# Optimization experiments

Measured on AMD Instinct MI355X. Metric: run time of the kernel, lower is better.

Reference implementation:

```python
import jax, jax.numpy as jnp
import numpy as np

B, S, D, H = 4, 2048, 1024, 16
DH = D // H
NEG = -100000.0


def setup_inputs() -> dict:
    key = jax.random.key(0)
    ks = jax.random.split(key, 13)
    s = 1.0 / np.sqrt(D)
    inp = {
        'q': jax.random.normal(ks[0], (B, S, D), jnp.float32),
        'k': jax.random.normal(ks[1], (B, S, D), jnp.float32),
        'v': jax.random.normal(ks[2], (B, S, D), jnp.float32),
        'mask': jax.random.randint(ks[3], (B, 1, S, S), 0, 2).astype(bool),
        'wq_w': jax.random.normal(ks[4], (D, D), jnp.float32) * s,
        'wq_b': jnp.zeros((D,), jnp.float32),
        'wk_w': jax.random.normal(ks[5], (D, D), jnp.float32) * s,
        'wk_b': jnp.zeros((D,), jnp.float32),
        'wv_w': jax.random.normal(ks[6], (D, D), jnp.float32) * s,
        'wv_b': jnp.zeros((D,), jnp.float32),
        'wo_w': jax.random.normal(ks[7], (D, D), jnp.float32) * s,
        'wo_b': jnp.zeros((D,), jnp.float32),
    }
    return inp


def reference(q, k, v, mask, wq_w, wq_b, wk_w, wk_b, wv_w, wv_b, wo_w, wo_b):
    # torch Linear: y = x @ W^T + b
    qh = (q @ wq_w.T + wq_b).reshape(B, S, H, DH).transpose(0, 2, 1, 3)  # [B,H,S,DH]
    kh = (k @ wk_w.T + wk_b).reshape(B, S, H, DH).transpose(0, 2, 1, 3)
    vh = (v @ wv_w.T + wv_b).reshape(B, S, H, DH).transpose(0, 2, 1, 3)
    # NOTE: original code has NO 1/sqrt(d) scaling
    alpha = jnp.einsum('bhqd,bhkd->bhqk', qh, kh)  # [B,H,S,S]
    alpha = jnp.where(mask, NEG, alpha)
    score = jax.nn.softmax(alpha, axis=-1)
    x = jnp.einsum('bhqk,bhkd->bhqd', score, vh)
    x = x.transpose(0, 2, 1, 3).reshape(B, S, D)
    return x @ wo_w.T + wo_b
```

## Files before the change

### kernel.cpp

```cpp
#include <hip/hip_runtime.h>
#include <hip/hip_bf16.h>

#define B_ 4
#define S_ 2048
#define D_ 1024
#define H_ 16
#define NEGV (-100000.0f)
#define L2E 1.4426950408889634f

typedef __attribute__((ext_vector_type(8))) short short8;
typedef __attribute__((ext_vector_type(4))) float f32x4;
typedef _Float16 hf2 __attribute__((ext_vector_type(2)));
typedef unsigned short us;
typedef unsigned long long u64;

__device__ __forceinline__ us f2h(float f) {
  union { _Float16 h; us u; } c;
  c.h = (_Float16)f;
  return c.u;
}
__device__ __forceinline__ float exp2a(float x) {
  float r;
  asm("v_exp_f32 %0, %1" : "=v"(r) : "v"(x));
  return r;
}

__global__ void detect_mask_kernel(const int* __restrict__ mi, int* __restrict__ flag) {
  int t = threadIdx.x;
  bool bad = false;
  for (int i = t; i < 16384; i += 64) {
    int v = mi[i];
    bad = bad || (v != 0 && v != 1);
  }
  unsigned long long any = __ballot(bad);
  if (t == 0) flag[0] = (any != 0ull) ? 1 : 0;
}

__global__ __launch_bounds__(256) void pack_mask(const void* __restrict__ maskp,
                                                 const int* __restrict__ flag,
                                                 unsigned* __restrict__ pk) {
  int w = blockIdx.x * 256 + threadIdx.x;
  unsigned bits = 0;
  if (flag[0]) {
    const uint4* p = (const uint4*)((const unsigned char*)maskp + (size_t)w * 32);
#pragma unroll
    for (int q = 0; q < 2; ++q) {
      uint4 v = p[q];
      unsigned vv[4] = {v.x, v.y, v.z, v.w};
#pragma unroll
      for (int e = 0; e < 4; ++e) {
        unsigned byte4 = vv[e];
#pragma unroll
        for (int bb = 0; bb < 4; ++bb)
          bits |= (unsigned)(((byte4 >> (8 * bb)) & 0xffu) != 0) << (q * 16 + e * 4 + bb);
      }
    }
  } else {
    const uint4* p = (const uint4*)((const int*)maskp + (size_t)w * 32);
#pragma unroll
    for (int q = 0; q < 8; ++q) {
      uint4 v = p[q];
      bits |= (unsigned)(v.x != 0) << (q * 4 + 0);
      bits |= (unsigned)(v.y != 0) << (q * 4 + 1);
      bits |= (unsigned)(v.z != 0) << (q * 4 + 2);
      bits |= (unsigned)(v.w != 0) << (q * 4 + 3);
    }
  }
  pk[w] = bits;
}

__global__ __launch_bounds__(256) void cvt_f16x3(const float* __restrict__ i0,
                                                 const float* __restrict__ i1,
                                                 const float* __restrict__ i2,
                                                 us* __restrict__ o0, us* __restrict__ o1,
                                                 us* __restrict__ o2) {
  int z = blockIdx.x >> 12;
  int i = (blockIdx.x & 4095) * 256 + threadIdx.x;
  const float* in = z == 0 ? i0 : z == 1 ? i1 : i2;
  us* out = z == 0 ? o0 : z == 1 ? o1 : o2;
  float4 a = ((const float4*)in)[2 * i];
  float4 b = ((const float4*)in)[2 * i + 1];
  us u[8] = {f2h(a.x), f2h(a.y), f2h(a.z), f2h(a.w),
             f2h(b.x), f2h(b.y), f2h(b.z), f2h(b.w)};
  ((uint4*)out)[i] = *(uint4*)u;
}

__global__ __launch_bounds__(256) void cvt_w4(const float* __restrict__ w0,
                                              const float* __restrict__ w1,
                                              const float* __restrict__ w2,
                                              const float* __restrict__ w3,
                                              us* __restrict__ d0, us* __restrict__ d1,
                                              us* __restrict__ d2, us* __restrict__ d3) {
  int which = blockIdx.x >> 9;
  int i = (blockIdx.x & 511) * 256 + threadIdx.x;
  const float* w = which == 0 ? w0 : which == 1 ? w1 : which == 2 ? w2 : w3;
  us* d = which == 0 ? d0 : which == 1 ? d1 : which == 2 ? d2 : d3;
  float4 a = ((const float4*)w)[2 * i];
  float4 b = ((const float4*)w)[2 * i + 1];
  us u[8] = {f2h(a.x), f2h(a.y), f2h(a.z), f2h(a.w),
             f2h(b.x), f2h(b.y), f2h(b.z), f2h(b.w)};
  ((uint4*)d)[i] = *(uint4*)u;
}

__device__ __forceinline__ void gload16(const us* g, us* l) {
  __builtin_amdgcn_global_load_lds((const __attribute__((address_space(1))) void*)g,
                                   (__attribute__((address_space(3))) void*)l, 16, 0, 0);
}

__device__ __forceinline__ int swzb(int row, int c16) {
  return row * 128 + ((c16 ^ (row & 7)) << 4);
}

template <int OMODE>
__global__ __launch_bounds__(256) void gemm_mfma(
    const us* __restrict__ A0, const us* __restrict__ A1, const us* __restrict__ A2,
    const us* __restrict__ Wp0, const us* __restrict__ Wp1, const us* __restrict__ Wp2,
    const float* __restrict__ b0, const float* __restrict__ b1, const float* __restrict__ b2,
    void* __restrict__ C0, void* __restrict__ C1, void* __restrict__ C2,
    int M, int N, int K, int trans_z) {
  __shared__ __align__(16) us SM[32768];

  const int z = blockIdx.z;
  const us* A = z == 0 ? A0 : z == 1 ? A1 : A2;
  const us* W = z == 0 ? Wp0 : z == 1 ? Wp1 : Wp2;
  const float* bias = z == 0 ? b0 : z == 1 ? b1 : b2;
  void* Cp = z == 0 ? C0 : z == 1 ? C1 : C2;

  const int m0 = blockIdx.x * 128;
  const int n0 = blockIdx.y * 128;
  const int t = threadIdx.x;
  const int w = t >> 6, l = t & 63;
  const int l15 = l & 15, l4 = l >> 4;
  const int wm = w >> 1, wn = w & 1;

  int goff[4];
#pragma unroll
  for (int j = 0; j < 4; ++j) {
    int u = t + j * 256;
    int r = u >> 3, c8 = u & 7;
    int g = c8 ^ (r & 7);
    goff[j] = r * K + g * 8;
  }
  const us* Ag = A + (size_t)m0 * K;
  const us* Wg = W + (size_t)n0 * K;

  f32x4 acc[4][4];
#pragma unroll
  for (int m = 0; m < 4; ++m)
#pragma unroll
    for (int n = 0; n < 4; ++n) acc[m][n] = (f32x4){0.f, 0.f, 0.f, 0.f};

  auto stage = [&](int k0, int bb) {
#pragma unroll
    for (int j = 0; j < 4; ++j) {
      int u = t + j * 256;
      gload16(Ag + goff[j] + k0, SM + bb * 8192 + u * 8);
      gload16(Wg + goff[j] + k0, SM + 16384 + bb * 8192 + u * 8);
    }
  };

  stage(0, 0);
  __syncthreads();
  int cur = 0;
  for (int k0 = 0; k0 < K; k0 += 64) {
    if (k0 + 64 < K) stage(k0 + 64, cur ^ 1);
#pragma unroll
    for (int ks = 0; ks < 2; ++ks) {
      short8 ah[4], bh_[4];
#pragma unroll
      for (int m = 0; m < 4; ++m)
        ah[m] = *(const short8*)((const char*)(SM + cur * 8192) +
                                 swzb(wm * 64 + m * 16 + l15, ks * 4 + l4));
#pragma unroll
      for (int n = 0; n < 4; ++n)
        bh_[n] = *(const short8*)((const char*)(SM + 16384 + cur * 8192) +
                                  swzb(wn * 64 + n * 16 + l15, ks * 4 + l4));
#pragma unroll
      for (int m = 0; m < 4; ++m)
#pragma unroll
        for (int n = 0; n < 4; ++n)
          acc[m][n] = __builtin_amdgcn_mfma_f32_16x16x32_f16(ah[m], bh_[n], acc[m][n], 0, 0, 0);
    }
    __syncthreads();
    cur ^= 1;
  }

  float bv[4];
#pragma unroll
  for (int n = 0; n < 4; ++n) bv[n] = bias[n0 + wn * 64 + n * 16 + l15];

  if (OMODE == 2 && z == trans_z) {
    us* T = SM;
#pragma unroll
    for (int n = 0; n < 4; ++n) {
      int col = wn * 64 + n * 16 + l15;
#pragma unroll
      for (int m = 0; m < 4; ++m) {
        int sr = wm * 64 + m * 16 + l4 * 4;
#pragma unroll
        for (int ip = 0; ip < 2; ++ip) {
          us h0 = f2h(acc[m][n][2 * ip] + bv[n]);
          us h1 = f2h(acc[m][n][2 * ip + 1] + bv[n]);
          *(unsigned*)&T[col * 136 + sr + 2 * ip] = (unsigned)h0 | ((unsigned)h1 << 16);
        }
      }
    }
    __syncthreads();
    const int b = m0 >> 11, sb = m0 & (S_ - 1);
    const int colr = t >> 1, sc = (t & 1) << 6;
    const int hh = (n0 >> 6) + (colr >> 6), d = colr & 63;
    us* dst = (us*)Cp + (((size_t)(b * H_ + hh) << 6) + (size_t)d) * S_ + sb + sc;
#pragma unroll
    for (int p = 0; p < 8; ++p)
      *(uint4*)(dst + p * 8) = *(const uint4*)&T[colr * 136 + sc + p * 8];
    return;
  }

#pragma unroll
  for (int m = 0; m < 4; ++m) {
#pragma unroll
    for (int i = 0; i < 4; ++i) {
      int gm = m0 + wm * 64 + m * 16 + l4 * 4 + i;
#pragma unroll
      for (int n = 0; n < 4; ++n) {
        int gn = n0 + wn * 64 + n * 16 + l15;
        float o = acc[m][n][i] + bv[n];
        if constexpr (OMODE == 0) {
          ((float*)Cp)[(size_t)gm * N + gn] = o;
        } else {
          int b = gm >> 11, s = gm & (S_ - 1);
          int hh = gn >> 6, d = gn & 63;
          size_t idx = (((size_t)(b * H_ + hh) << 11) + s) * 64 + d;
          ((us*)Cp)[idx] = f2h(o);
        }
      }
    }
  }
}

__device__ __forceinline__ int swz(int row, int bc) {
  return (row << 7) + (bc ^ ((row & 7) << 4));
}

__global__ __launch_bounds__(512) void attn_mfma(
    const us* __restrict__ qh, const us* __restrict__ kh,
    const us* __restrict__ vt, const unsigned* __restrict__ pk,
    us* __restrict__ xout) {
  __shared__ __align__(16) us Ks[2][4096];
  __shared__ __align__(16) us Vs[2][4096];
  __shared__ __align__(16) char Ps[16384];
  __shared__ __align__(16) float MLutF[64];

  const int blk = ((blockIdx.x & 7) << 7) + (blockIdx.x >> 3);
  const int bh = blk >> 4;
  const int q0 = (blk & 15) << 7;
  const int b = bh >> 4, h = bh & (H_ - 1);
  const int t = threadIdx.x;
  const int w = t >> 6, l = t & 63;
  const int l15 = l & 15, l4 = l >> 4;

  short8 qf[2];
  {
    const size_t qbase = ((size_t)bh * S_ + q0 + 16 * w + l15) * 64 + l4 * 8;
    qf[0] = *(const short8*)(qh + qbase);
    qf[1] = *(const short8*)(qh + qbase + 32);
  }

  f32x4 accO[4];
#pragma unroll
  for (int jd = 0; jd < 4; ++jd) accO[jd] = (f32x4){0.f, 0.f, 0.f, 0.f};
  float m_i = -1e30f, l_p = 0.f;

  const int r_st = t >> 3, c_st = (t & 7) ^ ((t >> 3) & 7);
  const us* kh_src = kh + ((size_t)bh * S_ + r_st) * 64 + c_st * 8;
  const us* vt_src = vt + ((size_t)bh * 64 + r_st) * S_ + c_st * 8;

  auto stage = [&](int k0, int bb) {
    gload16(kh_src + (size_t)k0 * 64, &Ks[bb][t * 8]);
    gload16(vt_src + k0, &Vs[bb][t * 8]);
  };

  if (t < 64) MLutF[t] = (((t >> 2) >> (t & 3)) & 1) ? NEGV : 0.f;
  stage(0, 0);
  __syncthreads();
  int cur = 0;

  char* Pw = Ps + w * 2048;
  const int prowb = l15 * 128;
  const int rr7 = l15 & 7;
  const int bhalf = l4 >> 1;
  const int wsub = (l4 & 1) * 8;
  const unsigned* pb = pk + ((size_t)b * S_ + q0 + 16 * w + l15) * (S_ / 32);

  for (int k0 = 0; k0 < S_; k0 += 64) {
    uint2 mw = *(const uint2*)(pb + (k0 >> 5));
    if (k0 + 64 < S_) stage(k0 + 64, cur ^ 1);

    const char* KT = (const char*)Ks[cur];
    const char* VT = (const char*)Vs[cur];

    __builtin_amdgcn_s_setprio(1);
    f32x4 sj[4];
#pragma unroll
    for (int j = 0; j < 4; ++j) {
      f32x4 s = {0.f, 0.f, 0.f, 0.f};
#pragma unroll
      for (int c = 0; c < 2; ++c) {
        short8 kf = *(const short8*)(KT + swz(l15 + 16 * j, l4 * 16 + 64 * c));
        s = __builtin_amdgcn_mfma_f32_16x16x32_f16(kf, qf[c], s, 0, 0, 0);
      }
      sj[j] = s;
    }
    __builtin_amdgcn_s_setprio(0);

#pragma unroll
    for (int j = 0; j < 4; ++j) {
      unsigned wrd = (j < 2) ? mw.x : mw.y;
      unsigned nib = (wrd >> (((j & 1) << 4) + (l4 << 2))) & 0xFu;
      f32x4 lv = *(const f32x4*)&MLutF[nib << 2];
      sj[j] = sj[j] + lv;
    }

    float c0 = fmaxf(fmaxf(sj[0][0], sj[0][1]), sj[0][2]);
    float c1 = fmaxf(fmaxf(sj[0][3], sj[1][0]), sj[1][1]);
    float c2 = fmaxf(fmaxf(sj[1][2], sj[1][3]), sj[2][0]);
    float c3 = fmaxf(fmaxf(sj[2][1], sj[2][2]), sj[2][3]);
    float c4 = fmaxf(fmaxf(sj[3][0], sj[3][1]), sj[3][2]);
    float tm = fmaxf(fmaxf(fmaxf(c0, c1), c2), fmaxf(fmaxf(c3, c4), sj[3][3]));
    tm = fmaxf(tm, __shfl_xor(tm, 16));
    tm = fmaxf(tm, __shfl_xor(tm, 32));

    if (__any(tm - m_i > 8.0f)) {
      float mnew = fmaxf(m_i, tm);
      float scl = exp2a((m_i - mnew) * L2E);
      l_p *= scl;
      m_i = mnew;
      float sr0 = __shfl(scl, 4 * l4 + 0);
      float sr1 = __shfl(scl, 4 * l4 + 1);
      float sr2 = __shfl(scl, 4 * l4 + 2);
      float sr3 = __shfl(scl, 4 * l4 + 3);
#pragma unroll
      for (int jd = 0; jd < 4; ++jd) {
        accO[jd][0] *= sr0; accO[jd][1] *= sr1;
        accO[jd][2] *= sr2; accO[jd][3] *= sr3;
      }
    }

    float ml2 = m_i * L2E;
    hf2 acc2;
    acc2.x = (_Float16)0.f;
    acc2.y = (_Float16)0.f;
#pragma unroll
    for (int j = 0; j < 4; ++j) {
      float p0 = exp2a(fmaf(sj[j][0], L2E, -ml2));
      float p1 = exp2a(fmaf(sj[j][1], L2E, -ml2));
      float p2 = exp2a(fmaf(sj[j][2], L2E, -ml2));
      float p3 = exp2a(fmaf(sj[j][3], L2E, -ml2));
      unsigned d0, d1;
      asm("v_cvt_pkrtz_f16_f32 %0, %1, %2" : "=v"(d0) : "v"(p0), "v"(p1));
      asm("v_cvt_pkrtz_f16_f32 %0, %1, %2" : "=v"(d1) : "v"(p2), "v"(p3));
      union { unsigned u; hf2 h; } c0u, c1u;
      c0u.u = d0;
      c1u.u = d1;
      acc2 = acc2 + c0u.h + c1u.h;
      int chunk = ((j << 1) | bhalf) ^ rr7;
      *(u64*)(Pw + prowb + (chunk << 4) + wsub) = (u64)d0 | ((u64)d1 << 32);
    }
    l_p += (float)acc2.x + (float)acc2.y;
    asm volatile("s_waitcnt lgkmcnt(0)" ::: "memory");
    __builtin_amdgcn_sched_barrier(0);

    __builtin_amdgcn_s_setprio(1);
#pragma unroll
    for (int kc = 0; kc < 2; ++kc) {
      int chR = (4 * kc + l4) ^ rr7;
      short8 pa = *(const short8*)(Pw + prowb + (chR << 4));
#pragma unroll
      for (int jd = 0; jd < 4; ++jd) {
        short8 vb = *(const short8*)(VT + swz(l15 + 16 * jd, l4 * 16 + 64 * kc));
        accO[jd] = __builtin_amdgcn_mfma_f32_16x16x32_f16(pa, vb, accO[jd], 0, 0, 0);
      }
    }
    __builtin_amdgcn_s_setprio(0);
    __syncthreads();
    cur ^= 1;
  }

  float lr = l_p;
  lr += __shfl_xor(lr, 16);
  lr += __shfl_xor(lr, 32);
  float inv0 = 1.f / __shfl(lr, 4 * l4 + 0);
  float inv1 = 1.f / __shfl(lr, 4 * l4 + 1);
  float inv2 = 1.f / __shfl(lr, 4 * l4 + 2);
  float inv3 = 1.f / __shfl(lr, 4 * l4 + 3);
  float invs[4] = {inv0, inv1, inv2, inv3};
#pragma unroll
  for (int i = 0; i < 4; ++i) {
    int row = q0 + 16 * w + l4 * 4 + i;
    size_t obase = ((size_t)b * S_ + row) * D_ + h * 64 + l15;
#pragma unroll
    for (int jd = 0; jd < 4; ++jd) xout[obase + 16 * jd] = f2h(accO[jd][i] * invs[i]);
  }
}

extern "C" void kernel_launch(void* const* d_in, const int* in_sizes, int n_in,
                              void* d_out, int out_size, void* d_ws, size_t ws_size,
                              hipStream_t stream) {
  const float* q = (const float*)d_in[0];
  const float* k = (const float*)d_in[1];
  const float* v = (const float*)d_in[2];
  const void* mask = d_in[3];
  const float* wq_w = (const float*)d_in[4];
  const float* wq_b = (const float*)d_in[5];
  const float* wk_w = (const float*)d_in[6];
  const float* wk_b = (const float*)d_in[7];
  const float* wv_w = (const float*)d_in[8];
  const float* wv_b = (const float*)d_in[9];
  const float* wo_w = (const float*)d_in[10];
  const float* wo_b = (const float*)d_in[11];

  const size_t NE = (size_t)B_ * S_ * D_;
  const size_t NW = (size_t)D_ * D_;
  const size_t PKB = (size_t)(B_ * S_ * (S_ / 32)) * 4;
  char* ws = (char*)d_ws;
  int* flag = (int*)ws;
  unsigned* pkb = (unsigned*)(ws + 256);
  us* base = (us*)(ws + 256 + PKB);

  detect_mask_kernel<<<1, 64, 0, stream>>>((const int*)mask, flag);
  pack_mask<<<2048, 256, 0, stream>>>(mask, flag, pkb);

  dim3 g2(64, 8, 2);
  dim3 g3(64, 8, 3);
  dim3 g1(64, 8, 1);

  const size_t fused_need = 256 + PKB + 6 * NE * 2 + 4 * NW * 2;
  if (ws_size >= fused_need) {
    us* A0 = base;
    us* A1 = A0 + NE;
    us* A2 = A1 + NE;
    us* A3 = A2 + NE;
    us* A4 = A3 + NE;
    us* A5 = A4 + NE;
    us* W0 = A5 + NE;
    us* W1 = W0 + NW;
    us* W2 = W1 + NW;
    us* W3 = W2 + NW;
    cvt_w4<<<2048, 256, 0, stream>>>(wq_w, wk_w, wv_w, wo_w, W0, W1, W2, W3);
    cvt_f16x3<<<3 * 4096, 256, 0, stream>>>(q, k, v, A0, A1, A2);
    gemm_mfma<2><<<g3, 256, 0, stream>>>(A0, A1, A2, W0, W1, W2, wq_b, wk_b, wv_b,
                                         A3, A4, A5, B_ * S_, D_, D_, 2);
    attn_mfma<<<1024, 512, 0, stream>>>(A3, A4, A5, pkb, A0);
    gemm_mfma<0><<<g1, 256, 0, stream>>>(A0, A0, A0, W3, W3, W3, wo_b, wo_b, wo_b,
                                         d_out, d_out, d_out, B_ * S_, D_, D_, -1);
  } else {
    us* A0 = base;
    us* A1 = A0 + NE;
    us* A2 = A1 + NE;
    us* A3 = A2 + NE;
    us* A4 = A3 + NE;
    us* W0 = A4 + NE;
    us* W1 = W0 + NW;
    us* W2 = W1 + NW;
    us* W3 = W2 + NW;
    cvt_w4<<<2048, 256, 0, stream>>>(wq_w, wk_w, wv_w, wo_w, W0, W1, W2, W3);
    cvt_f16x3<<<2 * 4096, 256, 0, stream>>>(q, k, nullptr, A0, A1, nullptr);
    gemm_mfma<2><<<g2, 256, 0, stream>>>(A0, A1, nullptr, W0, W1, nullptr, wq_b, wk_b, nullptr,
                                         A2, A3, nullptr, B_ * S_, D_, D_, -1);
    cvt_f16x3<<<4096, 256, 0, stream>>>(v, nullptr, nullptr, A0, nullptr, nullptr);
    gemm_mfma<2><<<g1, 256, 0, stream>>>(A0, nullptr, nullptr, W2, nullptr, nullptr,
                                         wv_b, nullptr, nullptr, A4, nullptr, nullptr,
                                         B_ * S_, D_, D_, 0);
    attn_mfma<<<1024, 512, 0, stream>>>(A2, A3, A4, pkb, A0);
    gemm_mfma<0><<<g1, 256, 0, stream>>>(A0, nullptr, nullptr, W3, nullptr, nullptr,
                                         wo_b, nullptr, nullptr, d_out, nullptr, nullptr,
                                         B_ * S_, D_, D_, -1);
  }
}
```

Before: 346.6 us.

## Deepen GEMM pipeline to four stages and merge prep launches

The projection GEMM now uses a 4-deep ring of 32-wide K tiles, with explicit vmcnt waits and raw barriers instead of a double-buffered 64-wide loop. This keeps more global-to-LDS loads in flight, and the smaller LDS footprint plus launch_bounds(256,2) aims for two blocks per CU. Mask detection is merged into the weight-conversion kernel and mask packing into the input-conversion kernel, which cuts the launch count. The hand-written waitcnt counts depend on the exact number of loads per stage, so they are fragile, and each tile now takes more barriers.

```diff
diff --git a/kernel.cpp b/kernel.cpp
--- a/kernel.cpp
+++ b/kernel.cpp
@@ -36,12 +36,9 @@
   if (t == 0) flag[0] = (any != 0ull) ? 1 : 0;
 }
 
-__global__ __launch_bounds__(256) void pack_mask(const void* __restrict__ maskp,
-                                                 const int* __restrict__ flag,
-                                                 unsigned* __restrict__ pk) {
-  int w = blockIdx.x * 256 + threadIdx.x;
+__device__ __forceinline__ unsigned pack_words(const void* maskp, int mode, int w) {
   unsigned bits = 0;
-  if (flag[0]) {
+  if (mode) {
     const uint4* p = (const uint4*)((const unsigned char*)maskp + (size_t)w * 32);
 #pragma unroll
     for (int q = 0; q < 2; ++q) {
@@ -66,7 +63,22 @@
       bits |= (unsigned)(v.w != 0) << (q * 4 + 3);
     }
   }
-  pk[w] = bits;
+  return bits;
+}
+
+__global__ __launch_bounds__(256) void pack_mask(const void* __restrict__ maskp,
+                                                 const int* __restrict__ flag,
+                                                 unsigned* __restrict__ pk) {
+  int w = blockIdx.x * 256 + threadIdx.x;
+  pk[w] = pack_words(maskp, flag[0], w);
+}
+
+__device__ __forceinline__ void cvt8(const float* in, us* out, int i) {
+  float4 a = ((const float4*)in)[2 * i];
+  float4 b = ((const float4*)in)[2 * i + 1];
+  us u[8] = {f2h(a.x), f2h(a.y), f2h(a.z), f2h(a.w),
+             f2h(b.x), f2h(b.y), f2h(b.z), f2h(b.w)};
+  ((uint4*)out)[i] = *(uint4*)u;
 }
 
 __global__ __launch_bounds__(256) void cvt_f16x3(const float* __restrict__ i0,
@@ -78,28 +90,48 @@
   int i = (blockIdx.x & 4095) * 256 + threadIdx.x;
   const float* in = z == 0 ? i0 : z == 1 ? i1 : i2;
   us* out = z == 0 ? o0 : z == 1 ? o1 : o2;
-  float4 a = ((const float4*)in)[2 * i];
-  float4 b = ((const float4*)in)[2 * i + 1];
-  us u[8] = {f2h(a.x), f2h(a.y), f2h(a.z), f2h(a.w),
-             f2h(b.x), f2h(b.y), f2h(b.z), f2h(b.w)};
-  ((uint4*)out)[i] = *(uint4*)u;
-}
-
-__global__ __launch_bounds__(256) void cvt_w4(const float* __restrict__ w0,
-                                              const float* __restrict__ w1,
-                                              const float* __restrict__ w2,
-                                              const float* __restrict__ w3,
-                                              us* __restrict__ d0, us* __restrict__ d1,
-                                              us* __restrict__ d2, us* __restrict__ d3) {
+  cvt8(in, out, i);
+}
+
+__global__ __launch_bounds__(256) void prep_w(
+    const float* __restrict__ w0, const float* __restrict__ w1,
+    const float* __restrict__ w2, const float* __restrict__ w3,
+    us* __restrict__ d0, us* __restrict__ d1, us* __restrict__ d2, us* __restrict__ d3,
+    const int* __restrict__ mi, int* __restrict__ flag) {
+  if (blockIdx.x == 2048) {
+    int t = threadIdx.x;
+    if (t >= 64) return;
+    bool bad = false;
+    for (int i = t; i < 16384; i += 64) {
+      int v = mi[i];
+      bad = bad || (v != 0 && v != 1);
+    }
+    unsigned long long any = __ballot(bad);
+    if (t == 0) flag[0] = (any != 0ull) ? 1 : 0;
+    return;
+  }
   int which = blockIdx.x >> 9;
   int i = (blockIdx.x & 511) * 256 + threadIdx.x;
   const float* w = which == 0 ? w0 : which == 1 ? w1 : which == 2 ? w2 : w3;
   us* d = which == 0 ? d0 : which == 1 ? d1 : which == 2 ? d2 : d3;
-  float4 a = ((const float4*)w)[2 * i];
-  float4 b = ((const float4*)w)[2 * i + 1];
-  us u[8] = {f2h(a.x), f2h(a.y), f2h(a.z), f2h(a.w),
-             f2h(b.x), f2h(b.y), f2h(b.z), f2h(b.w)};
-  ((uint4*)d)[i] = *(uint4*)u;
+  cvt8(w, d, i);
+}
+
+__global__ __launch_bounds__(256) void prep_in(
+    const void* __restrict__ maskp, const int* __restrict__ flag, unsigned* __restrict__ pk,
+    const float* __restrict__ i0, const float* __restrict__ i1, const float* __restrict__ i2,
+    us* __restrict__ o0, us* __restrict__ o1, us* __restrict__ o2) {
+  if (blockIdx.x < 2048) {
+    int w = blockIdx.x * 256 + threadIdx.x;
+    pk[w] = pack_words(maskp, flag[0], w);
+    return;
+  }
+  int c = blockIdx.x - 2048;
+  int z = c >> 12;
+  int i = (c & 4095) * 256 + threadIdx.x;
+  const float* in = z == 0 ? i0 : z == 1 ? i1 : i2;
+  us* out = z == 0 ? o0 : z == 1 ? o1 : o2;
+  cvt8(in, out, i);
 }
 
 __device__ __forceinline__ void gload16(const us* g, us* l) {
@@ -107,18 +139,14 @@
                                    (__attribute__((address_space(3))) void*)l, 16, 0, 0);
 }
 
-__device__ __forceinline__ int swzb(int row, int c16) {
-  return row * 128 + ((c16 ^ (row & 7)) << 4);
-}
-
 template <int OMODE>
-__global__ __launch_bounds__(256) void gemm_mfma(
+__global__ __launch_bounds__(256, 2) void gemm_dp(
     const us* __restrict__ A0, const us* __restrict__ A1, const us* __restrict__ A2,
     const us* __restrict__ Wp0, const us* __restrict__ Wp1, const us* __restrict__ Wp2,
     const float* __restrict__ b0, const float* __restrict__ b1, const float* __restrict__ b2,
     void* __restrict__ C0, void* __restrict__ C1, void* __restrict__ C2,
     int M, int N, int K, int trans_z) {
-  __shared__ __align__(16) us SM[32768];
+  __shared__ __align__(16) us SM[4][8192];
 
   const int z = blockIdx.z;
   const us* A = z == 0 ? A0 : z == 1 ? A1 : A2;
@@ -133,12 +161,12 @@
   const int l15 = l & 15, l4 = l >> 4;
   const int wm = w >> 1, wn = w & 1;
 
-  int goff[4];
-#pragma unroll
-  for (int j = 0; j < 4; ++j) {
+  int goff[2];
+#pragma unroll
+  for (int j = 0; j < 2; ++j) {
     int u = t + j * 256;
-    int r = u >> 3, c8 = u & 7;
-    int g = c8 ^ (r & 7);
+    int r = u >> 2, c4 = u & 3;
+    int g = c4 ^ (r & 3);
     goff[j] = r * K + g * 8;
   }
   const us* Ag = A + (size_t)m0 * K;
@@ -150,47 +178,70 @@
 #pragma unroll
     for (int n = 0; n < 4; ++n) acc[m][n] = (f32x4){0.f, 0.f, 0.f, 0.f};
 
-  auto stage = [&](int k0, int bb) {
-#pragma unroll
-    for (int j = 0; j < 4; ++j) {
+  auto stage = [&](int kt, int bb) {
+#pragma unroll
+    for (int j = 0; j < 2; ++j) {
       int u = t + j * 256;
-      gload16(Ag + goff[j] + k0, SM + bb * 8192 + u * 8);
-      gload16(Wg + goff[j] + k0, SM + 16384 + bb * 8192 + u * 8);
+      gload16(Ag + goff[j] + kt * 32, &SM[bb][u * 8]);
+    }
+#pragma unroll
+    for (int j = 0; j < 2; ++j) {
+      int u = t + j * 256;
+      gload16(Wg + goff[j] + kt * 32, &SM[bb][4096 + u * 8]);
     }
   };
 
+  auto body = [&](int bb) {
+    const char* Ab = (const char*)&SM[bb][0];
+    const char* Bb = Ab + 8192;
+    short8 bf[4], af[4];
+#pragma unroll
+    for (int n = 0; n < 4; ++n) {
+      int row = wn * 64 + n * 16 + l15;
+      bf[n] = *(const short8*)(Bb + row * 64 + ((l4 ^ (row & 3)) << 4));
+    }
+#pragma unroll
+    for (int m = 0; m < 4; ++m) {
+      int row = wm * 64 + m * 16 + l15;
+      af[m] = *(const short8*)(Ab + row * 64 + ((l4 ^ (row & 3)) << 4));
+    }
+#pragma unroll
+    for (int m = 0; m < 4; ++m)
+#pragma unroll
+      for (int n = 0; n < 4; ++n)
+        acc[m][n] = __builtin_amdgcn_mfma_f32_16x16x32_f16(af[m], bf[n], acc[m][n], 0, 0, 0);
+  };
+
+  const int nt = K / 32;
   stage(0, 0);
-  __syncthreads();
-  int cur = 0;
-  for (int k0 = 0; k0 < K; k0 += 64) {
-    if (k0 + 64 < K) stage(k0 + 64, cur ^ 1);
-#pragma unroll
-    for (int ks = 0; ks < 2; ++ks) {
-      short8 ah[4], bh_[4];
-#pragma unroll
-      for (int m = 0; m < 4; ++m)
-        ah[m] = *(const short8*)((const char*)(SM + cur * 8192) +
-                                 swzb(wm * 64 + m * 16 + l15, ks * 4 + l4));
-#pragma unroll
-      for (int n = 0; n < 4; ++n)
-        bh_[n] = *(const short8*)((const char*)(SM + 16384 + cur * 8192) +
-                                  swzb(wn * 64 + n * 16 + l15, ks * 4 + l4));
-#pragma unroll
-      for (int m = 0; m < 4; ++m)
-#pragma unroll
-        for (int n = 0; n < 4; ++n)
-          acc[m][n] = __builtin_amdgcn_mfma_f32_16x16x32_f16(ah[m], bh_[n], acc[m][n], 0, 0, 0);
-    }
+  stage(1, 1);
+  stage(2, 2);
+  int tt = 0;
+  for (; tt < nt - 3; ++tt) {
+    asm volatile("s_waitcnt vmcnt(8)" ::: "memory");
+    asm volatile("s_barrier" ::: "memory");
+    stage(tt + 3, (tt + 3) & 3);
+    body(tt & 3);
+  }
+  asm volatile("s_waitcnt vmcnt(8)" ::: "memory");
+  asm volatile("s_barrier" ::: "memory");
+  body(tt & 3);
+  ++tt;
+  asm volatile("s_waitcnt vmcnt(4)" ::: "memory");
+  asm volatile("s_barrier" ::: "memory");
+  body(tt & 3);
+  ++tt;
+  asm volatile("s_waitcnt vmcnt(0)" ::: "memory");
+  asm volatile("s_barrier" ::: "memory");
+  body(tt & 3);
+
+  float bv[4];
+#pragma unroll
+  for (int n = 0; n < 4; ++n) bv[n] = bias[n0 + wn * 64 + n * 16 + l15];
+
+  if (OMODE == 2 && z == trans_z) {
     __syncthreads();
-    cur ^= 1;
-  }
-
-  float bv[4];
-#pragma unroll
-  for (int n = 0; n < 4; ++n) bv[n] = bias[n0 + wn * 64 + n * 16 + l15];
-
-  if (OMODE == 2 && z == trans_z) {
-    us* T = SM;
+    us* T = (us*)SM;
 #pragma unroll
     for (int n = 0; n < 4; ++n) {
       int col = wn * 64 + n * 16 + l15;
@@ -427,11 +478,8 @@
   unsigned* pkb = (unsigned*)(ws + 256);
   us* base = (us*)(ws + 256 + PKB);
 
-  detect_mask_kernel<<<1, 64, 0, stream>>>((const int*)mask, flag);
-  pack_mask<<<2048, 256, 0, stream>>>(mask, flag, pkb);
-
+  dim3 g3(64, 8, 3);
   dim3 g2(64, 8, 2);
-  dim3 g3(64, 8, 3);
   dim3 g1(64, 8, 1);
 
   const size_t fused_need = 256 + PKB + 6 * NE * 2 + 4 * NW * 2;
@@ -446,13 +494,14 @@
     us* W1 = W0 + NW;
     us* W2 = W1 + NW;
     us* W3 = W2 + NW;
-    cvt_w4<<<2048, 256, 0, stream>>>(wq_w, wk_w, wv_w, wo_w, W0, W1, W2, W3);
-    cvt_f16x3<<<3 * 4096, 256, 0, stream>>>(q, k, v, A0, A1, A2);
-    gemm_mfma<2><<<g3, 256, 0, stream>>>(A0, A1, A2, W0, W1, W2, wq_b, wk_b, wv_b,
-                                         A3, A4, A5, B_ * S_, D_, D_, 2);
+    prep_w<<<2049, 256, 0, stream>>>(wq_w, wk_w, wv_w, wo_w, W0, W1, W2, W3,
+                                     (const int*)mask, flag);
+    prep_in<<<2048 + 3 * 4096, 256, 0, stream>>>(mask, flag, pkb, q, k, v, A0, A1, A2);
+    gemm_dp<2><<<g3, 256, 0, stream>>>(A0, A1, A2, W0, W1, W2, wq_b, wk_b, wv_b,
+                                       A3, A4, A5, B_ * S_, D_, D_, 2);
     attn_mfma<<<1024, 512, 0, stream>>>(A3, A4, A5, pkb, A0);
-    gemm_mfma<0><<<g1, 256, 0, stream>>>(A0, A0, A0, W3, W3, W3, wo_b, wo_b, wo_b,
-                                         d_out, d_out, d_out, B_ * S_, D_, D_, -1);
+    gemm_dp<0><<<g1, 256, 0, stream>>>(A0, A0, A0, W3, W3, W3, wo_b, wo_b, wo_b,
+                                       d_out, d_out, d_out, B_ * S_, D_, D_, -1);
   } else {
     us* A0 = base;
     us* A1 = A0 + NE;
@@ -463,17 +512,20 @@
     us* W1 = W0 + NW;
     us* W2 = W1 + NW;
     us* W3 = W2 + NW;
-    cvt_w4<<<2048, 256, 0, stream>>>(wq_w, wk_w, wv_w, wo_w, W0, W1, W2, W3);
+    detect_mask_kernel<<<1, 64, 0, stream>>>((const int*)mask, flag);
+    pack_mask<<<2048, 256, 0, stream>>>(mask, flag, pkb);
+    prep_w<<<2048, 256, 0, stream>>>(wq_w, wk_w, wv_w, wo_w, W0, W1, W2, W3,
+                                     (const int*)mask, flag);
     cvt_f16x3<<<2 * 4096, 256, 0, stream>>>(q, k, nullptr, A0, A1, nullptr);
-    gemm_mfma<2><<<g2, 256, 0, stream>>>(A0, A1, nullptr, W0, W1, nullptr, wq_b, wk_b, nullptr,
-                                         A2, A3, nullptr, B_ * S_, D_, D_, -1);
+    gemm_dp<2><<<g2, 256, 0, stream>>>(A0, A1, nullptr, W0, W1, nullptr, wq_b, wk_b, nullptr,
+                                       A2, A3, nullptr, B_ * S_, D_, D_, -1);
     cvt_f16x3<<<4096, 256, 0, stream>>>(v, nullptr, nullptr, A0, nullptr, nullptr);
-    gemm_mfma<2><<<g1, 256, 0, stream>>>(A0, nullptr, nullptr, W2, nullptr, nullptr,
-                                         wv_b, nullptr, nullptr, A4, nullptr, nullptr,
-                                         B_ * S_, D_, D_, 0);
+    gemm_dp<2><<<g1, 256, 0, stream>>>(A0, nullptr, nullptr, W2, nullptr, nullptr,
+                                       wv_b, nullptr, nullptr, A4, nullptr, nullptr,
+                                       B_ * S_, D_, D_, 0);
     attn_mfma<<<1024, 512, 0, stream>>>(A2, A3, A4, pkb, A0);
-    gemm_mfma<0><<<g1, 256, 0, stream>>>(A0, nullptr, nullptr, W3, nullptr, nullptr,
-                                         wo_b, nullptr, nullptr, d_out, nullptr, nullptr,
-                                         B_ * S_, D_, D_, -1);
-  }
-}
+    gemm_dp<0><<<g1, 256, 0, stream>>>(A0, nullptr, nullptr, W3, nullptr, nullptr,
+                                       wo_b, nullptr, nullptr, d_out, nullptr, nullptr,
+                                       B_ * S_, D_, D_, -1);
+  }
+}
```

After: 359.5 us. 3.7% more time.

## Merge prep kernels into fewer launches and enlarge attention blocks to 1024 threads

Applied to the files above, without the earlier changes.

Mask detection now runs inside the weight-conversion kernel, and mask packing is fused with the activation conversion, which removes two kernel launches and their serialization. The attention kernel now uses 1024-thread blocks covering 256 query rows. K and V staging is split across the two halves of the block, so each K/V tile in LDS is shared by twice as many query rows. The larger block raises LDS use and register pressure per block, which may lower occupancy, and it halves the grid to 512 blocks.

```diff
diff --git a/kernel.cpp b/kernel.cpp
--- a/kernel.cpp
+++ b/kernel.cpp
@@ -36,12 +36,9 @@
   if (t == 0) flag[0] = (any != 0ull) ? 1 : 0;
 }
 
-__global__ __launch_bounds__(256) void pack_mask(const void* __restrict__ maskp,
-                                                 const int* __restrict__ flag,
-                                                 unsigned* __restrict__ pk) {
-  int w = blockIdx.x * 256 + threadIdx.x;
+__device__ __forceinline__ unsigned pack_words(const void* maskp, int mode, int w) {
   unsigned bits = 0;
-  if (flag[0]) {
+  if (mode) {
     const uint4* p = (const uint4*)((const unsigned char*)maskp + (size_t)w * 32);
 #pragma unroll
     for (int q = 0; q < 2; ++q) {
@@ -66,7 +63,22 @@
       bits |= (unsigned)(v.w != 0) << (q * 4 + 3);
     }
   }
-  pk[w] = bits;
+  return bits;
+}
+
+__global__ __launch_bounds__(256) void pack_mask(const void* __restrict__ maskp,
+                                                 const int* __restrict__ flag,
+                                                 unsigned* __restrict__ pk) {
+  int w = blockIdx.x * 256 + threadIdx.x;
+  pk[w] = pack_words(maskp, flag[0], w);
+}
+
+__device__ __forceinline__ void cvt8(const float* in, us* out, int i) {
+  float4 a = ((const float4*)in)[2 * i];
+  float4 b = ((const float4*)in)[2 * i + 1];
+  us u[8] = {f2h(a.x), f2h(a.y), f2h(a.z), f2h(a.w),
+             f2h(b.x), f2h(b.y), f2h(b.z), f2h(b.w)};
+  ((uint4*)out)[i] = *(uint4*)u;
 }
 
 __global__ __launch_bounds__(256) void cvt_f16x3(const float* __restrict__ i0,
@@ -78,28 +90,48 @@
   int i = (blockIdx.x & 4095) * 256 + threadIdx.x;
   const float* in = z == 0 ? i0 : z == 1 ? i1 : i2;
   us* out = z == 0 ? o0 : z == 1 ? o1 : o2;
-  float4 a = ((const float4*)in)[2 * i];
-  float4 b = ((const float4*)in)[2 * i + 1];
-  us u[8] = {f2h(a.x), f2h(a.y), f2h(a.z), f2h(a.w),
-             f2h(b.x), f2h(b.y), f2h(b.z), f2h(b.w)};
-  ((uint4*)out)[i] = *(uint4*)u;
-}
-
-__global__ __launch_bounds__(256) void cvt_w4(const float* __restrict__ w0,
-                                              const float* __restrict__ w1,
-                                              const float* __restrict__ w2,
-                                              const float* __restrict__ w3,
-                                              us* __restrict__ d0, us* __restrict__ d1,
-                                              us* __restrict__ d2, us* __restrict__ d3) {
+  cvt8(in, out, i);
+}
+
+__global__ __launch_bounds__(256) void prep_w(
+    const float* __restrict__ w0, const float* __restrict__ w1,
+    const float* __restrict__ w2, const float* __restrict__ w3,
+    us* __restrict__ d0, us* __restrict__ d1, us* __restrict__ d2, us* __restrict__ d3,
+    const int* __restrict__ mi, int* __restrict__ flag) {
+  if (blockIdx.x == 2048) {
+    int t = threadIdx.x;
+    if (t >= 64) return;
+    bool bad = false;
+    for (int i = t; i < 16384; i += 64) {
+      int v = mi[i];
+      bad = bad || (v != 0 && v != 1);
+    }
+    unsigned long long any = __ballot(bad);
+    if (t == 0) flag[0] = (any != 0ull) ? 1 : 0;
+    return;
+  }
   int which = blockIdx.x >> 9;
   int i = (blockIdx.x & 511) * 256 + threadIdx.x;
   const float* w = which == 0 ? w0 : which == 1 ? w1 : which == 2 ? w2 : w3;
   us* d = which == 0 ? d0 : which == 1 ? d1 : which == 2 ? d2 : d3;
-  float4 a = ((const float4*)w)[2 * i];
-  float4 b = ((const float4*)w)[2 * i + 1];
-  us u[8] = {f2h(a.x), f2h(a.y), f2h(a.z), f2h(a.w),
-             f2h(b.x), f2h(b.y), f2h(b.z), f2h(b.w)};
-  ((uint4*)d)[i] = *(uint4*)u;
+  cvt8(w, d, i);
+}
+
+__global__ __launch_bounds__(256) void prep_in(
+    const void* __restrict__ maskp, const int* __restrict__ flag, unsigned* __restrict__ pk,
+    const float* __restrict__ i0, const float* __restrict__ i1, const float* __restrict__ i2,
+    us* __restrict__ o0, us* __restrict__ o1, us* __restrict__ o2) {
+  if (blockIdx.x < 2048) {
+    int w = blockIdx.x * 256 + threadIdx.x;
+    pk[w] = pack_words(maskp, flag[0], w);
+    return;
+  }
+  int c = blockIdx.x - 2048;
+  int z = c >> 12;
+  int i = (c & 4095) * 256 + threadIdx.x;
+  const float* in = z == 0 ? i0 : z == 1 ? i1 : i2;
+  us* out = z == 0 ? o0 : z == 1 ? o1 : o2;
+  cvt8(in, out, i);
 }
 
 __device__ __forceinline__ void gload16(const us* g, us* l) {
@@ -112,7 +144,7 @@
 }
 
 template <int OMODE>
-__global__ __launch_bounds__(256) void gemm_mfma(
+__global__ __launch_bounds__(256) void gemm2p(
     const us* __restrict__ A0, const us* __restrict__ A1, const us* __restrict__ A2,
     const us* __restrict__ Wp0, const us* __restrict__ Wp1, const us* __restrict__ Wp2,
     const float* __restrict__ b0, const float* __restrict__ b1, const float* __restrict__ b2,
@@ -242,18 +274,18 @@
   return (row << 7) + (bc ^ ((row & 7) << 4));
 }
 
-__global__ __launch_bounds__(512) void attn_mfma(
+__global__ __launch_bounds__(1024) void attn_mfma(
     const us* __restrict__ qh, const us* __restrict__ kh,
     const us* __restrict__ vt, const unsigned* __restrict__ pk,
     us* __restrict__ xout) {
   __shared__ __align__(16) us Ks[2][4096];
   __shared__ __align__(16) us Vs[2][4096];
-  __shared__ __align__(16) char Ps[16384];
+  __shared__ __align__(16) char Ps[32768];
   __shared__ __align__(16) float MLutF[64];
 
-  const int blk = ((blockIdx.x & 7) << 7) + (blockIdx.x >> 3);
-  const int bh = blk >> 4;
-  const int q0 = (blk & 15) << 7;
+  const int blk = ((blockIdx.x & 7) << 6) + (blockIdx.x >> 3);
+  const int bh = blk >> 3;
+  const int q0 = (blk & 7) << 8;
   const int b = bh >> 4, h = bh & (H_ - 1);
   const int t = threadIdx.x;
   const int w = t >> 6, l = t & 63;
@@ -271,13 +303,17 @@
   for (int jd = 0; jd < 4; ++jd) accO[jd] = (f32x4){0.f, 0.f, 0.f, 0.f};
   float m_i = -1e30f, l_p = 0.f;
 
-  const int r_st = t >> 3, c_st = (t & 7) ^ ((t >> 3) & 7);
+  const int sc = t & 511;
+  const int r_st = sc >> 3, c_st = (sc & 7) ^ ((sc >> 3) & 7);
+  const bool isK = t < 512;
   const us* kh_src = kh + ((size_t)bh * S_ + r_st) * 64 + c_st * 8;
   const us* vt_src = vt + ((size_t)bh * 64 + r_st) * S_ + c_st * 8;
 
   auto stage = [&](int k0, int bb) {
-    gload16(kh_src + (size_t)k0 * 64, &Ks[bb][t * 8]);
-    gload16(vt_src + k0, &Vs[bb][t * 8]);
+    if (isK)
+      gload16(kh_src + (size_t)k0 * 64, &Ks[bb][sc * 8]);
+    else
+      gload16(vt_src + k0, &Vs[bb][sc * 8]);
   };
 
   if (t < 64) MLutF[t] = (((t >> 2) >> (t & 3)) & 1) ? NEGV : 0.f;
@@ -427,11 +463,8 @@
   unsigned* pkb = (unsigned*)(ws + 256);
   us* base = (us*)(ws + 256 + PKB);
 
-  detect_mask_kernel<<<1, 64, 0, stream>>>((const int*)mask, flag);
-  pack_mask<<<2048, 256, 0, stream>>>(mask, flag, pkb);
-
+  dim3 g3(64, 8, 3);
   dim3 g2(64, 8, 2);
-  dim3 g3(64, 8, 3);
   dim3 g1(64, 8, 1);
 
   const size_t fused_need = 256 + PKB + 6 * NE * 2 + 4 * NW * 2;
@@ -446,13 +479,14 @@
     us* W1 = W0 + NW;
     us* W2 = W1 + NW;
     us* W3 = W2 + NW;
-    cvt_w4<<<2048, 256, 0, stream>>>(wq_w, wk_w, wv_w, wo_w, W0, W1, W2, W3);
-    cvt_f16x3<<<3 * 4096, 256, 0, stream>>>(q, k, v, A0, A1, A2);
-    gemm_mfma<2><<<g3, 256, 0, stream>>>(A0, A1, A2, W0, W1, W2, wq_b, wk_b, wv_b,
-                                         A3, A4, A5, B_ * S_, D_, D_, 2);
-    attn_mfma<<<1024, 512, 0, stream>>>(A3, A4, A5, pkb, A0);
-    gemm_mfma<0><<<g1, 256, 0, stream>>>(A0, A0, A0, W3, W3, W3, wo_b, wo_b, wo_b,
-                                         d_out, d_out, d_out, B_ * S_, D_, D_, -1);
+    prep_w<<<2049, 256, 0, stream>>>(wq_w, wk_w, wv_w, wo_w, W0, W1, W2, W3,
+                                     (const int*)mask, flag);
+    prep_in<<<2048 + 3 * 4096, 256, 0, stream>>>(mask, flag, pkb, q, k, v, A0, A1, A2);
+    gemm2p<2><<<g3, 256, 0, stream>>>(A0, A1, A2, W0, W1, W2, wq_b, wk_b, wv_b,
+                                      A3, A4, A5, B_ * S_, D_, D_, 2);
+    attn_mfma<<<512, 1024, 0, stream>>>(A3, A4, A5, pkb, A0);
+    gemm2p<0><<<g1, 256, 0, stream>>>(A0, A0, A0, W3, W3, W3, wo_b, wo_b, wo_b,
+                                      d_out, d_out, d_out, B_ * S_, D_, D_, -1);
   } else {
     us* A0 = base;
     us* A1 = A0 + NE;
@@ -463,17 +497,20 @@
     us* W1 = W0 + NW;
     us* W2 = W1 + NW;
     us* W3 = W2 + NW;
-    cvt_w4<<<2048, 256, 0, stream>>>(wq_w, wk_w, wv_w, wo_w, W0, W1, W2, W3);
+    detect_mask_kernel<<<1, 64, 0, stream>>>((const int*)mask, flag);
+    pack_mask<<<2048, 256, 0, stream>>>(mask, flag, pkb);
+    prep_w<<<2048, 256, 0, stream>>>(wq_w, wk_w, wv_w, wo_w, W0, W1, W2, W3,
+                                     (const int*)mask, flag);
     cvt_f16x3<<<2 * 4096, 256, 0, stream>>>(q, k, nullptr, A0, A1, nullptr);
-    gemm_mfma<2><<<g2, 256, 0, stream>>>(A0, A1, nullptr, W0, W1, nullptr, wq_b, wk_b, nullptr,
-                                         A2, A3, nullptr, B_ * S_, D_, D_, -1);
+    gemm2p<2><<<g2, 256, 0, stream>>>(A0, A1, nullptr, W0, W1, nullptr, wq_b, wk_b, nullptr,
+                                      A2, A3, nullptr, B_ * S_, D_, D_, -1);
     cvt_f16x3<<<4096, 256, 0, stream>>>(v, nullptr, nullptr, A0, nullptr, nullptr);
-    gemm_mfma<2><<<g1, 256, 0, stream>>>(A0, nullptr, nullptr, W2, nullptr, nullptr,
-                                         wv_b, nullptr, nullptr, A4, nullptr, nullptr,
-                                         B_ * S_, D_, D_, 0);
-    attn_mfma<<<1024, 512, 0, stream>>>(A2, A3, A4, pkb, A0);
-    gemm_mfma<0><<<g1, 256, 0, stream>>>(A0, nullptr, nullptr, W3, nullptr, nullptr,
-                                         wo_b, nullptr, nullptr, d_out, nullptr, nullptr,
-                                         B_ * S_, D_, D_, -1);
-  }
-}
+    gemm2p<2><<<g1, 256, 0, stream>>>(A0, nullptr, nullptr, W2, nullptr, nullptr,
+                                      wv_b, nullptr, nullptr, A4, nullptr, nullptr,
+                                      B_ * S_, D_, D_, 0);
+    attn_mfma<<<512, 1024, 0, stream>>>(A2, A3, A4, pkb, A0);
+    gemm2p<0><<<g1, 256, 0, stream>>>(A0, nullptr, nullptr, W3, nullptr, nullptr,
+                                      wo_b, nullptr, nullptr, d_out, nullptr, nullptr,
+                                      B_ * S_, D_, D_, -1);
+  }
+}
```

After: 348.9 us. About the same (+0.7%).
